# Kernel optimization log

Measured on AMD Instinct MI355X. Metric: run time of the kernel, lower is better.

## Reference

```python
import jax, jax.numpy as jnp
import numpy as np


def setup_inputs() -> dict:
    key = jax.random.key(0)
    ks = jax.random.split(key, 8)
    B, N, C = 8, 4096, 128
    x = jax.random.normal(ks[0], (B, N, C), dtype=jnp.float32)
    spatial_pos = jax.random.randint(ks[1], (1, N, N), 0, 6, dtype=jnp.int32)
    sc = 1.0 / np.sqrt(C)
    W1 = jax.random.normal(ks[2], (C, C), dtype=jnp.float32) * sc
    b1 = jax.random.normal(ks[3], (C,), dtype=jnp.float32) * 0.01
    W2 = jax.random.normal(ks[4], (C, C // 8), dtype=jnp.float32) * sc
    b2 = jax.random.normal(ks[5], (C // 8,), dtype=jnp.float32) * 0.01
    Wb = jax.random.normal(ks[6], (C + C // 8, C), dtype=jnp.float32) * (1.0 / np.sqrt(C + C // 8))
    bb = jax.random.normal(ks[7], (C,), dtype=jnp.float32) * 0.01
    return {"x": x, "spatial_pos": spatial_pos, "W1": W1, "b1": b1,
            "W2": W2, "b2": b2, "Wb": Wb, "bb": bb}


def reference(x, spatial_pos, W1, b1, W2, b2, Wb, bb):
    # s=1, l=2: scale k=1 uses mask (spatial_pos <= 1), k=2 uses (spatial_pos == 2)
    sp = spatial_pos[0]                      # [N, N], batch-invariant
    m1 = (sp <= 1).astype(x.dtype)           # [N, N]
    m2 = (sp == 2).astype(x.dtype)           # [N, N]
    h1 = x @ W1 + b1                         # [B, N, C]
    h2 = x @ W2 + b2                         # [B, N, C//8]
    # torch.bmm(mask.expand(B,-1,-1), h) == einsum over shared mask
    f1 = jnp.einsum('ij,bjc->bic', m1, h1)   # [B, N, C]
    f2 = jnp.einsum('ij,bjc->bic', m2, h2)   # [B, N, C//8]
    feats = jnp.concatenate([f1, f2], axis=-1)  # [B, N, C + C//8]
    return feats @ Wb + bb                   # [B, N, output_dim]
```

## Files before the change

kernel.cpp:

```cpp
#include <hip/hip_runtime.h>
#include <stdint.h>

typedef unsigned short u16;
typedef __attribute__((ext_vector_type(8))) short short8;
typedef __attribute__((ext_vector_type(4))) float f32x4;

#define MFMA __builtin_amdgcn_mfma_f32_16x16x32_bf16

__device__ __forceinline__ u16 f2bf(float f) {
  union { float f; uint32_t u; } v; v.f = f;
  return (u16)((v.u + 0x7FFFu + ((v.u >> 16) & 1u)) >> 16);
}

#define GLOAD16(gp, lp) \
  __builtin_amdgcn_global_load_lds((const __attribute__((address_space(1))) uint32_t*)(gp), \
                                   (__attribute__((address_space(3))) uint32_t*)(lp), 16, 0, 0)

#define WS_H    0
#define WS_Q1   9502720
#define WS_Q2   9503232
#define WS_M1P  9503744
#define WS_M2P  11600896
#define WS_RS1  13698048
#define WS_RS2  13714432
#define WS_WSB  13730816

__global__ __launch_bounds__(256) void k0(const int* __restrict__ sp,
                                          unsigned long long* __restrict__ m1p,
                                          unsigned long long* __restrict__ m2p,
                                          float* __restrict__ rs1, float* __restrict__ rs2,
                                          const float* __restrict__ W1, const float* __restrict__ Wb,
                                          const float* __restrict__ b1, const float* __restrict__ b2,
                                          const float* __restrict__ W2,
                                          float* __restrict__ q1, float* __restrict__ q2,
                                          u16* __restrict__ wsbg) {
  const int tid = threadIdx.x;
  if (blockIdx.x < 1024) {
    int wave = tid >> 6, lane = tid & 63;
    int i = blockIdx.x * 4 + wave;
    const int* rowp = sp + (size_t)i * 4096;
    int c1 = 0, c2 = 0;
    for (int w = 0; w < 64; ++w) {
      int v = rowp[w * 64 + lane];
      unsigned long long bb1 = __ballot(v <= 1);
      unsigned long long bb2 = __ballot(v == 2);
      if (lane == 0) {
        m1p[(size_t)w * 4096 + i] = bb1;
        m2p[(size_t)w * 4096 + i] = bb2;
        c1 += __popcll(bb1);
        c2 += __popcll(bb2);
      }
    }
    if (lane == 0) { rs1[i] = (float)c1; rs2[i] = (float)c2; }
    return;
  }
  int idx = (int)(blockIdx.x - 1024) * 256 + tid;
  int a = idx >> 7, c = idx & 127;
  float acc = 0.f;
  for (int k = 0; k < 128; ++k) acc += W1[a * 128 + k] * Wb[k * 128 + c];
  wsbg[(((a >> 3) * 144) + c) * 8 + (a & 7)] = f2bf(acc);
  if (idx < 2048) {
    int k = idx >> 4, nn2 = idx & 15;
    wsbg[(((k >> 3) * 144) + 128 + nn2) * 8 + (k & 7)] = f2bf(W2[k * 16 + nn2]);
  }
  if (idx < 128) {
    float s1 = 0.f, s2 = 0.f;
    for (int k = 0; k < 128; ++k) s1 += b1[k] * Wb[k * 128 + idx];
    for (int k = 0; k < 16; ++k)  s2 += b2[k] * Wb[(128 + k) * 128 + idx];
    q1[idx] = s1; q2[idx] = s2;
  }
}

__global__ __launch_bounds__(256, 2) void kproj(const float* __restrict__ x,
                                                const u16* __restrict__ wsbg,
                                                u16* __restrict__ H) {
  __shared__ u16 wsb[18432];
  __shared__ u16 xs[64 * 136];
  __shared__ u16 hs[64 * 146];
  const int tid = threadIdx.x;
  const int bid = blockIdx.x;
  const int b = bid >> 6;
  const int kt = bid & 63;
  const size_t r0 = (size_t)b * 4096 + (size_t)kt * 64;

#pragma unroll
  for (int i = 0; i < 9; ++i)
    GLOAD16(wsbg + (i * 256 + tid) * 8, (char*)&wsb[0] + (i * 256 + tid) * 16);
  {
    const float* xp = x + (r0 + (tid >> 2)) * 128 + (tid & 3) * 32;
    u16* xd = xs + (tid >> 2) * 136 + (tid & 3) * 32;
#pragma unroll
    for (int i = 0; i < 4; ++i) {
      f32x4 a = ((const f32x4*)xp)[i * 2];
      f32x4 bq = ((const f32x4*)xp)[i * 2 + 1];
      short8 pk;
      pk[0] = (short)f2bf(a[0]); pk[1] = (short)f2bf(a[1]);
      pk[2] = (short)f2bf(a[2]); pk[3] = (short)f2bf(a[3]);
      pk[4] = (short)f2bf(bq[0]); pk[5] = (short)f2bf(bq[1]);
      pk[6] = (short)f2bf(bq[2]); pk[7] = (short)f2bf(bq[3]);
      *(short8*)(xd + i * 8) = pk;
    }
  }
  __syncthreads();

  const int w = tid >> 6, l = tid & 63, lr = l & 15, lg = l >> 4;
  f32x4 acc[9];
  f32x4 zz = {0.f, 0.f, 0.f, 0.f};
#pragma unroll
  for (int fn = 0; fn < 9; ++fn) acc[fn] = zz;
#pragma unroll
  for (int kf = 0; kf < 4; ++kf) {
    short8 af = *(const short8*)(xs + (w * 16 + lr) * 136 + kf * 32 + lg * 8);
#pragma unroll
    for (int fn = 0; fn < 9; ++fn) {
      short8 bf = *(const short8*)(wsb + (((kf * 4 + lg) * 144) + fn * 16 + lr) * 8);
      acc[fn] = MFMA(af, bf, acc[fn], 0, 0, 0);
    }
  }
  __syncthreads();
#pragma unroll
  for (int fn = 0; fn < 9; ++fn)
#pragma unroll
    for (int g = 0; g < 4; ++g)
      hs[(w * 16 + lg * 4 + g) * 146 + fn * 16 + lr] = f2bf(acc[fn][g]);
  __syncthreads();
  for (int i = 0; i < 5; ++i) {
    int e = i * 256 + tid;
    if (e < 1152) {
      int jbl = e / 144, n = e % 144;
      union { u16 s[8]; uint4 v; } pk;
#pragma unroll
      for (int r = 0; r < 8; ++r) pk.s[r] = hs[(jbl * 8 + r) * 146 + n];
      int kf = jbl >> 2, lgw = jbl & 3, fn = n >> 4, lrw = n & 15;
      size_t di = ((((size_t)kt * 2 + kf) * 8 + b) * 9 + fn) * 512 + (lgw * 16 + lrw) * 8;
      *(uint4*)(H + di) = pk.v;
    }
  }
}

__device__ __forceinline__ short8 expand_byte(uint32_t wd, int lgsh) {
  uint32_t b = (wd >> lgsh) & 0xFFu;
  uint32_t t = b * 0x8001u;
  union { uint32_t u[4]; short8 s; } r;
  r.u[0] = (t & 0x00010001u) * 0x3F80u;
  r.u[1] = (t & 0x00040004u) * 0x0FE0u;
  r.u[2] = (t & 0x00100010u) * 0x03F8u;
  r.u[3] = (t & 0x00400040u) * 0x00FEu;
  return r.s;
}

__global__ __launch_bounds__(1024, 4) void kb1(const u16* __restrict__ H,
                                               const char* __restrict__ M1b,
                                               const char* __restrict__ M2b,
                                               const float* __restrict__ rs1, const float* __restrict__ rs2,
                                               const float* __restrict__ q1, const float* __restrict__ q2,
                                               const float* __restrict__ Wb, const float* __restrict__ bb,
                                               float* __restrict__ out) {
  __shared__ u16 bt[3][18432];
  __shared__ u16 mkb[3][2048];
  __shared__ float f2pf[2][128][16];
  __shared__ u16 f2s[128 * 40];
  __shared__ u16 wb2s[4096];

  const int tid = threadIdx.x;
  const int bid = blockIdx.x;
  const int b = bid & 7;
  const int i0 = (bid >> 3) * 128;

  const int w = tid >> 6, l = tid & 63, lr = l & 15, lg = l >> 4;
  const int g = w >> 2, c = w & 3;
  const int fm2 = w & 7, kf2 = w >> 3;
  const int lgsh = lg * 8;

  auto choff = [&](int ch) -> uint32_t {
    int slab = (ch >= 1152) ? 1 : 0;
    int r = ch - slab * 1152;
    return (uint32_t)(slab * 73728 + (r < 576 ? b * 4608 + r * 8 : 36864 + b * 4608 + (r - 576) * 8));
  };
  const u16* pB0 = H + choff(tid);
  const u16* pB1 = H + choff(1024 + tid);
  const u16* pB2 = H + choff(tid < 256 ? 2048 + tid : 2048);
  const int dB0 = tid * 16, dB1 = (1024 + tid) * 16, dB2 = (2048 + tid) * 16;
  const int mc = tid - 256;
  const char* pM = (((mc >> 6) & 1) ? M2b : M1b) + (size_t)((mc >> 7) & 1) * 32768
                 + (size_t)i0 * 8 + (size_t)(mc & 63) * 16;
  const int dM = mc * 16;

#define STAGE(BUF) { \
    GLOAD16(pB0, (char*)&bt[BUF][0] + dB0); \
    GLOAD16(pB1, (char*)&bt[BUF][0] + dB1); \
    if (tid < 256) GLOAD16(pB2, (char*)&bt[BUF][0] + dB2); \
    else if (tid < 512) GLOAD16(pM, (char*)&mkb[BUF][0] + dM); \
    pB0 += 147456; pB1 += 147456; pB2 += 147456; pM += 65536; }

  const int fA0 = (c * 2 + 0) * 512 + l * 8;
  const int fA1 = (c * 2 + 1) * 512 + l * 8;
  const int fB0 = 4608 + fA0;
  const int fB1 = 4608 + fA1;
  const int fM  = kf2 * 4608 + 4096 + l * 8;

  f32x4 zz = {0.f, 0.f, 0.f, 0.f};
  f32x4 acc00 = zz, acc01 = zz, acc10 = zz, acc11 = zz;
  f32x4 acc2 = zz;

#define WAITV { if (w < 8) asm volatile("s_waitcnt vmcnt(3)" ::: "memory"); \
                else asm volatile("s_waitcnt vmcnt(2)" ::: "memory"); }

#define CKT(BUF, S) { \
    const u16* src_ = &bt[BUF][(S) * 9216]; \
    const char* mk_ = (const char*)&mkb[BUF][0] + (S) * 2048; \
    uint2 c0_ = *(const uint2*)(mk_ + ((g * 2 + 0) * 16 + lr) * 8); \
    uint2 c1_ = *(const uint2*)(mk_ + ((g * 2 + 1) * 16 + lr) * 8); \
    uint32_t c2_ = *(const uint32_t*)(mk_ + 1024 + (fm2 * 16 + lr) * 8 + kf2 * 4); \
    short8 bA0_ = *(const short8*)(src_ + fA0); \
    short8 bA1_ = *(const short8*)(src_ + fA1); \
    short8 bB0_ = *(const short8*)(src_ + fB0); \
    short8 bB1_ = *(const short8*)(src_ + fB1); \
    short8 bM_  = *(const short8*)(src_ + fM); \
    short8 e0x_ = expand_byte(c0_.x, lgsh), e0y_ = expand_byte(c0_.y, lgsh); \
    short8 e1x_ = expand_byte(c1_.x, lgsh), e1y_ = expand_byte(c1_.y, lgsh); \
    short8 e2v_ = expand_byte(c2_, lgsh); \
    __builtin_amdgcn_s_setprio(1); \
    acc00 = MFMA(e0x_, bA0_, acc00, 0, 0, 0); \
    acc01 = MFMA(e0x_, bA1_, acc01, 0, 0, 0); \
    acc00 = MFMA(e0y_, bB0_, acc00, 0, 0, 0); \
    acc01 = MFMA(e0y_, bB1_, acc01, 0, 0, 0); \
    acc10 = MFMA(e1x_, bA0_, acc10, 0, 0, 0); \
    acc11 = MFMA(e1x_, bA1_, acc11, 0, 0, 0); \
    acc10 = MFMA(e1y_, bB0_, acc10, 0, 0, 0); \
    acc11 = MFMA(e1y_, bB1_, acc11, 0, 0, 0); \
    acc2  = MFMA(e2v_, bM_, acc2, 0, 0, 0); \
    __builtin_amdgcn_s_setprio(0); }

#define COMPUTE2(BUF) { CKT(BUF, 0) CKT(BUF, 1) }

  STAGE(0);
  STAGE(1);

#pragma unroll
  for (int i = 0; i < 4; ++i) {
    int e = i * 1024 + tid;
    int r_ = e & 7, nn = (e >> 3) & 127, jb = e >> 10;
    int k = jb * 8 + r_;
    wb2s[e] = f2bf((k < 16) ? Wb[(128 + k) * 128 + nn] : 0.f);
  }

  for (int it = 0; it < 10; ++it) {
    WAITV; __builtin_amdgcn_s_barrier(); STAGE(2); COMPUTE2(0);
    WAITV; __builtin_amdgcn_s_barrier(); STAGE(0); COMPUTE2(1);
    WAITV; __builtin_amdgcn_s_barrier(); STAGE(1); COMPUTE2(2);
  }
  WAITV; __builtin_amdgcn_s_barrier(); COMPUTE2(0);
  { asm volatile("s_waitcnt vmcnt(0)" ::: "memory");
    __builtin_amdgcn_s_barrier(); COMPUTE2(1); }

#pragma unroll
  for (int gg = 0; gg < 4; ++gg)
    f2pf[kf2][fm2 * 16 + lg * 4 + gg][lr] = acc2[gg];
  __syncthreads();
#pragma unroll
  for (int j = 0; j < 2; ++j) {
    int e = j * 1024 + tid;
    int row = e >> 4, col = e & 15;
    f2s[row * 40 + col] = f2bf(f2pf[0][row][col] + f2pf[1][row][col]);
    f2s[row * 40 + 16 + col] = 0;
  }
  __syncthreads();

  short8 bw0 = *(const short8*)(wb2s + ((lg * 128) + (c * 2 + 0) * 16 + lr) * 8);
  short8 bw1 = *(const short8*)(wb2s + ((lg * 128) + (c * 2 + 1) * 16 + lr) * 8);
  {
    short8 af0 = *(const short8*)(f2s + ((g * 2 + 0) * 16 + lr) * 40 + lg * 8);
    short8 af1 = *(const short8*)(f2s + ((g * 2 + 1) * 16 + lr) * 40 + lg * 8);
    acc00 = MFMA(af0, bw0, acc00, 0, 0, 0);
    acc01 = MFMA(af0, bw1, acc01, 0, 0, 0);
    acc10 = MFMA(af1, bw0, acc10, 0, 0, 0);
    acc11 = MFMA(af1, bw1, acc11, 0, 0, 0);
  }

  const int col0 = (c * 2 + 0) * 16 + lr, col1 = (c * 2 + 1) * 16 + lr;
  const float q10 = q1[col0], q20 = q2[col0], bb0 = bb[col0];
  const float q11 = q1[col1], q21 = q2[col1], bb1 = bb[col1];
#pragma unroll
  for (int i = 0; i < 2; ++i) {
    f32x4 a0 = i ? acc10 : acc00;
    f32x4 a1 = i ? acc11 : acc01;
#pragma unroll
    for (int gg = 0; gg < 4; ++gg) {
      int row = (g * 2 + i) * 16 + lg * 4 + gg;
      float r1 = rs1[i0 + row], r2 = rs2[i0 + row];
      size_t obase = ((size_t)b * 4096 + i0 + row) * 128;
      out[obase + col0] = a0[gg] + r1 * q10 + r2 * q20 + bb0;
      out[obase + col1] = a1[gg] + r1 * q11 + r2 * q21 + bb1;
    }
  }
}

extern "C" void kernel_launch(void* const* d_in, const int* in_sizes, int n_in,
                              void* d_out, int out_size, void* d_ws, size_t ws_size,
                              hipStream_t stream) {
  const float* x  = (const float*)d_in[0];
  const int*   sp = (const int*)d_in[1];
  const float* W1 = (const float*)d_in[2];
  const float* b1 = (const float*)d_in[3];
  const float* W2 = (const float*)d_in[4];
  const float* b2 = (const float*)d_in[5];
  const float* Wb = (const float*)d_in[6];
  const float* bb = (const float*)d_in[7];
  float* out = (float*)d_out;
  char* ws = (char*)d_ws;

  u16* H = (u16*)(ws + WS_H);
  float* q1 = (float*)(ws + WS_Q1);
  float* q2 = (float*)(ws + WS_Q2);
  unsigned long long* m1p = (unsigned long long*)(ws + WS_M1P);
  unsigned long long* m2p = (unsigned long long*)(ws + WS_M2P);
  float* rs1 = (float*)(ws + WS_RS1);
  float* rs2 = (float*)(ws + WS_RS2);
  u16* wsbg = (u16*)(ws + WS_WSB);

  k0<<<1088, 256, 0, stream>>>(sp, m1p, m2p, rs1, rs2, W1, Wb, b1, b2, W2, q1, q2, wsbg);
  kproj<<<512, 256, 0, stream>>>(x, wsbg, H);
  kb1<<<256, 1024, 0, stream>>>(H, (const char*)m1p, (const char*)m2p,
                                rs1, rs2, q1, q2, Wb, bb, out);
}
```

Baseline: 91.99 us.

## Halve kb1 block to 512 threads with 4 row-tiles per wave and single k-slab stages

Restructures the main mask-times-H kernel to launch 512-thread blocks instead of 1024. Each wave now accumulates four 16-row tiles instead of two, and the f2 accumulation is done per-wave without a cross-wave reduction. Each pipeline stage now loads one k-slab instead of two, halving LDS buffers, and the loop runs 60 stages instead of 30. This raises per-wave register use and MFMA work per B-fragment load to improve reuse. The cost is fewer waves to hide latency and more barriers per unit of work.

```diff
diff --git a/kernel.cpp b/kernel.cpp
--- a/kernel.cpp
+++ b/kernel.cpp
@@ -149,16 +149,15 @@
   return r.s;
 }
 
-__global__ __launch_bounds__(1024, 4) void kb1(const u16* __restrict__ H,
-                                               const char* __restrict__ M1b,
-                                               const char* __restrict__ M2b,
-                                               const float* __restrict__ rs1, const float* __restrict__ rs2,
-                                               const float* __restrict__ q1, const float* __restrict__ q2,
-                                               const float* __restrict__ Wb, const float* __restrict__ bb,
-                                               float* __restrict__ out) {
-  __shared__ u16 bt[3][18432];
-  __shared__ u16 mkb[3][2048];
-  __shared__ float f2pf[2][128][16];
+__global__ __launch_bounds__(512, 4) void kb1(const u16* __restrict__ H,
+                                              const char* __restrict__ M1b,
+                                              const char* __restrict__ M2b,
+                                              const float* __restrict__ rs1, const float* __restrict__ rs2,
+                                              const float* __restrict__ q1, const float* __restrict__ q2,
+                                              const float* __restrict__ Wb, const float* __restrict__ bb,
+                                              float* __restrict__ out) {
+  __shared__ u16 bt[3][9216];
+  __shared__ u16 mkb[3][1024];
   __shared__ u16 f2s[128 * 40];
   __shared__ u16 wb2s[4096];
 
@@ -168,130 +167,144 @@
   const int i0 = (bid >> 3) * 128;
 
   const int w = tid >> 6, l = tid & 63, lr = l & 15, lg = l >> 4;
-  const int g = w >> 2, c = w & 3;
-  const int fm2 = w & 7, kf2 = w >> 3;
+  const int h = w >> 2, c = w & 3;
   const int lgsh = lg * 8;
 
-  auto choff = [&](int ch) -> uint32_t {
-    int slab = (ch >= 1152) ? 1 : 0;
-    int r = ch - slab * 1152;
-    return (uint32_t)(slab * 73728 + (r < 576 ? b * 4608 + r * 8 : 36864 + b * 4608 + (r - 576) * 8));
-  };
-  const u16* pB0 = H + choff(tid);
-  const u16* pB1 = H + choff(1024 + tid);
-  const u16* pB2 = H + choff(tid < 256 ? 2048 + tid : 2048);
-  const int dB0 = tid * 16, dB1 = (1024 + tid) * 16, dB2 = (2048 + tid) * 16;
-  const int mc = tid - 256;
-  const char* pM = (((mc >> 6) & 1) ? M2b : M1b) + (size_t)((mc >> 7) & 1) * 32768
-                 + (size_t)i0 * 8 + (size_t)(mc & 63) * 16;
-  const int dM = mc * 16;
+  const u16* pB0 = H + b * 4608 + (size_t)tid * 8;
+  const u16* pB1 = H + ((512 + tid) < 576 ? (b * 4608 + (size_t)(512 + tid) * 8)
+                                          : (36864 + b * 4608 + (size_t)(512 + tid - 576) * 8));
+  const u16* pB2 = H + 36864 + b * 4608 + (size_t)(448 + tid) * 8;
+  const int mc = tid - 128;
+  const char* pM = ((mc & 64) ? M2b : M1b) + (size_t)i0 * 8 + (size_t)(mc & 63) * 16;
+  const int dB0 = tid * 16, dB1 = (512 + tid) * 16, dB2 = (1024 + tid) * 16;
+  const int dM = ((mc >> 6) & 1) * 1024 + (mc & 63) * 16;
 
 #define STAGE(BUF) { \
     GLOAD16(pB0, (char*)&bt[BUF][0] + dB0); \
     GLOAD16(pB1, (char*)&bt[BUF][0] + dB1); \
-    if (tid < 256) GLOAD16(pB2, (char*)&bt[BUF][0] + dB2); \
-    else if (tid < 512) GLOAD16(pM, (char*)&mkb[BUF][0] + dM); \
-    pB0 += 147456; pB1 += 147456; pB2 += 147456; pM += 65536; }
-
-  const int fA0 = (c * 2 + 0) * 512 + l * 8;
-  const int fA1 = (c * 2 + 1) * 512 + l * 8;
-  const int fB0 = 4608 + fA0;
-  const int fB1 = 4608 + fA1;
-  const int fM  = kf2 * 4608 + 4096 + l * 8;
+    if (tid < 128) GLOAD16(pB2, (char*)&bt[BUF][0] + dB2); \
+    else if (tid < 256) GLOAD16(pM, (char*)&mkb[BUF][0] + dM); \
+    pB0 += 73728; pB1 += 73728; pB2 += 73728; pM += 32768; }
+
+  const int f00 = (c * 2 + 0) * 512 + l * 8;
+  const int f01 = (c * 2 + 1) * 512 + l * 8;
+  const int f10 = 4608 + f00;
+  const int f11 = 4608 + f01;
+  const int fm0 = 4096 + l * 8;
+  const int fm1 = 4608 + 4096 + l * 8;
 
   f32x4 zz = {0.f, 0.f, 0.f, 0.f};
-  f32x4 acc00 = zz, acc01 = zz, acc10 = zz, acc11 = zz;
+  f32x4 a00 = zz, a01 = zz, a10 = zz, a11 = zz, a20 = zz, a21 = zz, a30 = zz, a31 = zz;
   f32x4 acc2 = zz;
 
-#define WAITV { if (w < 8) asm volatile("s_waitcnt vmcnt(3)" ::: "memory"); \
+#define WAITV { if (w < 4) asm volatile("s_waitcnt vmcnt(3)" ::: "memory"); \
                 else asm volatile("s_waitcnt vmcnt(2)" ::: "memory"); }
 
-#define CKT(BUF, S) { \
-    const u16* src_ = &bt[BUF][(S) * 9216]; \
-    const char* mk_ = (const char*)&mkb[BUF][0] + (S) * 2048; \
-    uint2 c0_ = *(const uint2*)(mk_ + ((g * 2 + 0) * 16 + lr) * 8); \
-    uint2 c1_ = *(const uint2*)(mk_ + ((g * 2 + 1) * 16 + lr) * 8); \
-    uint32_t c2_ = *(const uint32_t*)(mk_ + 1024 + (fm2 * 16 + lr) * 8 + kf2 * 4); \
-    short8 bA0_ = *(const short8*)(src_ + fA0); \
-    short8 bA1_ = *(const short8*)(src_ + fA1); \
-    short8 bB0_ = *(const short8*)(src_ + fB0); \
-    short8 bB1_ = *(const short8*)(src_ + fB1); \
-    short8 bM_  = *(const short8*)(src_ + fM); \
+#define COMPUTE(BUF) { \
+    const u16* src_ = &bt[BUF][0]; \
+    const char* mk_ = (const char*)&mkb[BUF][0]; \
+    uint2 c0_ = *(const uint2*)(mk_ + ((4 * h + 0) * 16 + lr) * 8); \
+    uint2 c1_ = *(const uint2*)(mk_ + ((4 * h + 1) * 16 + lr) * 8); \
+    uint2 c2_ = *(const uint2*)(mk_ + ((4 * h + 2) * 16 + lr) * 8); \
+    uint2 c3_ = *(const uint2*)(mk_ + ((4 * h + 3) * 16 + lr) * 8); \
+    uint2 cm_ = *(const uint2*)(mk_ + 1024 + (w * 16 + lr) * 8); \
+    short8 b00_ = *(const short8*)(src_ + f00); \
+    short8 b01_ = *(const short8*)(src_ + f01); \
+    short8 b10_ = *(const short8*)(src_ + f10); \
+    short8 b11_ = *(const short8*)(src_ + f11); \
+    short8 bm0_ = *(const short8*)(src_ + fm0); \
+    short8 bm1_ = *(const short8*)(src_ + fm1); \
     short8 e0x_ = expand_byte(c0_.x, lgsh), e0y_ = expand_byte(c0_.y, lgsh); \
     short8 e1x_ = expand_byte(c1_.x, lgsh), e1y_ = expand_byte(c1_.y, lgsh); \
-    short8 e2v_ = expand_byte(c2_, lgsh); \
+    short8 e2x_ = expand_byte(c2_.x, lgsh), e2y_ = expand_byte(c2_.y, lgsh); \
+    short8 e3x_ = expand_byte(c3_.x, lgsh), e3y_ = expand_byte(c3_.y, lgsh); \
+    short8 emx_ = expand_byte(cm_.x, lgsh), emy_ = expand_byte(cm_.y, lgsh); \
     __builtin_amdgcn_s_setprio(1); \
-    acc00 = MFMA(e0x_, bA0_, acc00, 0, 0, 0); \
-    acc01 = MFMA(e0x_, bA1_, acc01, 0, 0, 0); \
-    acc00 = MFMA(e0y_, bB0_, acc00, 0, 0, 0); \
-    acc01 = MFMA(e0y_, bB1_, acc01, 0, 0, 0); \
-    acc10 = MFMA(e1x_, bA0_, acc10, 0, 0, 0); \
-    acc11 = MFMA(e1x_, bA1_, acc11, 0, 0, 0); \
-    acc10 = MFMA(e1y_, bB0_, acc10, 0, 0, 0); \
-    acc11 = MFMA(e1y_, bB1_, acc11, 0, 0, 0); \
-    acc2  = MFMA(e2v_, bM_, acc2, 0, 0, 0); \
+    a00 = MFMA(e0x_, b00_, a00, 0, 0, 0); \
+    a01 = MFMA(e0x_, b01_, a01, 0, 0, 0); \
+    a00 = MFMA(e0y_, b10_, a00, 0, 0, 0); \
+    a01 = MFMA(e0y_, b11_, a01, 0, 0, 0); \
+    a10 = MFMA(e1x_, b00_, a10, 0, 0, 0); \
+    a11 = MFMA(e1x_, b01_, a11, 0, 0, 0); \
+    a10 = MFMA(e1y_, b10_, a10, 0, 0, 0); \
+    a11 = MFMA(e1y_, b11_, a11, 0, 0, 0); \
+    a20 = MFMA(e2x_, b00_, a20, 0, 0, 0); \
+    a21 = MFMA(e2x_, b01_, a21, 0, 0, 0); \
+    a20 = MFMA(e2y_, b10_, a20, 0, 0, 0); \
+    a21 = MFMA(e2y_, b11_, a21, 0, 0, 0); \
+    a30 = MFMA(e3x_, b00_, a30, 0, 0, 0); \
+    a31 = MFMA(e3x_, b01_, a31, 0, 0, 0); \
+    a30 = MFMA(e3y_, b10_, a30, 0, 0, 0); \
+    a31 = MFMA(e3y_, b11_, a31, 0, 0, 0); \
+    acc2 = MFMA(emx_, bm0_, acc2, 0, 0, 0); \
+    acc2 = MFMA(emy_, bm1_, acc2, 0, 0, 0); \
     __builtin_amdgcn_s_setprio(0); }
 
-#define COMPUTE2(BUF) { CKT(BUF, 0) CKT(BUF, 1) }
+#define PHASE(BUF, BUF2) { WAITV; __builtin_amdgcn_s_barrier(); STAGE(BUF2); COMPUTE(BUF) }
 
   STAGE(0);
   STAGE(1);
 
 #pragma unroll
-  for (int i = 0; i < 4; ++i) {
-    int e = i * 1024 + tid;
+  for (int i = 0; i < 8; ++i) {
+    int e = i * 512 + tid;
     int r_ = e & 7, nn = (e >> 3) & 127, jb = e >> 10;
     int k = jb * 8 + r_;
     wb2s[e] = f2bf((k < 16) ? Wb[(128 + k) * 128 + nn] : 0.f);
   }
 
-  for (int it = 0; it < 10; ++it) {
-    WAITV; __builtin_amdgcn_s_barrier(); STAGE(2); COMPUTE2(0);
-    WAITV; __builtin_amdgcn_s_barrier(); STAGE(0); COMPUTE2(1);
-    WAITV; __builtin_amdgcn_s_barrier(); STAGE(1); COMPUTE2(2);
-  }
-  WAITV; __builtin_amdgcn_s_barrier(); COMPUTE2(0);
+  for (int it = 0; it < 20; ++it) {
+    PHASE(0, 2);
+    PHASE(1, 0);
+    PHASE(2, 1);
+  }
+  PHASE(0, 2);
+  PHASE(1, 0);
+  { WAITV; __builtin_amdgcn_s_barrier(); COMPUTE(2) }
   { asm volatile("s_waitcnt vmcnt(0)" ::: "memory");
-    __builtin_amdgcn_s_barrier(); COMPUTE2(1); }
-
+    __builtin_amdgcn_s_barrier(); COMPUTE(0) }
+
+#pragma unroll
+  for (int j = 0; j < 4; ++j) {
+    int e = tid * 4 + j;
+    f2s[(e >> 4) * 40 + 16 + (e & 15)] = 0;
+  }
 #pragma unroll
   for (int gg = 0; gg < 4; ++gg)
-    f2pf[kf2][fm2 * 16 + lg * 4 + gg][lr] = acc2[gg];
-  __syncthreads();
-#pragma unroll
-  for (int j = 0; j < 2; ++j) {
-    int e = j * 1024 + tid;
-    int row = e >> 4, col = e & 15;
-    f2s[row * 40 + col] = f2bf(f2pf[0][row][col] + f2pf[1][row][col]);
-    f2s[row * 40 + 16 + col] = 0;
-  }
+    f2s[(w * 16 + lg * 4 + gg) * 40 + lr] = f2bf(acc2[gg]);
   __syncthreads();
 
   short8 bw0 = *(const short8*)(wb2s + ((lg * 128) + (c * 2 + 0) * 16 + lr) * 8);
   short8 bw1 = *(const short8*)(wb2s + ((lg * 128) + (c * 2 + 1) * 16 + lr) * 8);
   {
-    short8 af0 = *(const short8*)(f2s + ((g * 2 + 0) * 16 + lr) * 40 + lg * 8);
-    short8 af1 = *(const short8*)(f2s + ((g * 2 + 1) * 16 + lr) * 40 + lg * 8);
-    acc00 = MFMA(af0, bw0, acc00, 0, 0, 0);
-    acc01 = MFMA(af0, bw1, acc01, 0, 0, 0);
-    acc10 = MFMA(af1, bw0, acc10, 0, 0, 0);
-    acc11 = MFMA(af1, bw1, acc11, 0, 0, 0);
+    short8 af0 = *(const short8*)(f2s + ((4 * h + 0) * 16 + lr) * 40 + lg * 8);
+    short8 af1 = *(const short8*)(f2s + ((4 * h + 1) * 16 + lr) * 40 + lg * 8);
+    short8 af2 = *(const short8*)(f2s + ((4 * h + 2) * 16 + lr) * 40 + lg * 8);
+    short8 af3 = *(const short8*)(f2s + ((4 * h + 3) * 16 + lr) * 40 + lg * 8);
+    a00 = MFMA(af0, bw0, a00, 0, 0, 0);
+    a01 = MFMA(af0, bw1, a01, 0, 0, 0);
+    a10 = MFMA(af1, bw0, a10, 0, 0, 0);
+    a11 = MFMA(af1, bw1, a11, 0, 0, 0);
+    a20 = MFMA(af2, bw0, a20, 0, 0, 0);
+    a21 = MFMA(af2, bw1, a21, 0, 0, 0);
+    a30 = MFMA(af3, bw0, a30, 0, 0, 0);
+    a31 = MFMA(af3, bw1, a31, 0, 0, 0);
   }
 
   const int col0 = (c * 2 + 0) * 16 + lr, col1 = (c * 2 + 1) * 16 + lr;
   const float q10 = q1[col0], q20 = q2[col0], bb0 = bb[col0];
   const float q11 = q1[col1], q21 = q2[col1], bb1 = bb[col1];
 #pragma unroll
-  for (int i = 0; i < 2; ++i) {
-    f32x4 a0 = i ? acc10 : acc00;
-    f32x4 a1 = i ? acc11 : acc01;
+  for (int i = 0; i < 4; ++i) {
+    f32x4 v0 = (i == 0) ? a00 : (i == 1) ? a10 : (i == 2) ? a20 : a30;
+    f32x4 v1 = (i == 0) ? a01 : (i == 1) ? a11 : (i == 2) ? a21 : a31;
 #pragma unroll
     for (int gg = 0; gg < 4; ++gg) {
-      int row = (g * 2 + i) * 16 + lg * 4 + gg;
+      int row = (4 * h + i) * 16 + lg * 4 + gg;
       float r1 = rs1[i0 + row], r2 = rs2[i0 + row];
       size_t obase = ((size_t)b * 4096 + i0 + row) * 128;
-      out[obase + col0] = a0[gg] + r1 * q10 + r2 * q20 + bb0;
-      out[obase + col1] = a1[gg] + r1 * q11 + r2 * q21 + bb1;
+      out[obase + col0] = v0[gg] + r1 * q10 + r2 * q20 + bb0;
+      out[obase + col1] = v1[gg] + r1 * q11 + r2 * q21 + bb1;
     }
   }
 }
@@ -321,6 +334,6 @@
 
   k0<<<1088, 256, 0, stream>>>(sp, m1p, m2p, rs1, rs2, W1, Wb, b1, b2, W2, q1, q2, wsbg);
   kproj<<<512, 256, 0, stream>>>(x, wsbg, H);
-  kb1<<<256, 1024, 0, stream>>>(H, (const char*)m1p, (const char*)m2p,
-                                rs1, rs2, q1, q2, Wb, bb, out);
-}
+  kb1<<<256, 512, 0, stream>>>(H, (const char*)m1p, (const char*)m2p,
+                               rs1, rs2, q1, q2, Wb, bb, out);
+}
```

Result: slower. 100.5 us (+9.3%).
